# Kernel optimization log

Measured on AMD Instinct MI355X. Metric: run time of the kernel, lower is better.

## Reference

```python
import jax, jax.numpy as jnp
import numpy as np

B, S, E, H = 4, 4096, 1024, 128

def setup_inputs() -> dict:
    key = jax.random.key(0)
    kx, kk, kq, kv = jax.random.split(key, 4)
    x = jax.random.normal(kx, (B, S, E), dtype=jnp.float32)
    # torch nn.Linear weights are [out_features, in_features]
    Wk = jax.random.normal(kk, (H, E), dtype=jnp.float32) * (E ** -0.5)
    Wq = jax.random.normal(kq, (H, E), dtype=jnp.float32) * (E ** -0.5)
    Wv = jax.random.normal(kv, (H, E), dtype=jnp.float32) * (E ** -0.5)
    return {"x": x, "Wk": Wk, "Wq": Wq, "Wv": Wv}

def reference(x, Wk, Wq, Wv):
    # projections: y = x @ W.T  (bias-free nn.Linear)
    k = jnp.einsum('bse,he->bsh', x, Wk)
    q = jnp.einsum('bse,he->bsh', x, Wq)
    v = jnp.einsum('bse,he->bsh', x, Wv)
    emb = x.shape[-1]
    # scores scaled by embedding_size**-0.5 (as in the source, not head_size)
    scores = jnp.einsum('bqh,bkh->bqk', q, k) * (emb ** -0.5)  # [B,S,S]
    # causal mask: positions j > i get -inf
    i = jnp.arange(scores.shape[-2])[:, None]
    j = jnp.arange(scores.shape[-1])[None, :]
    scores = jnp.where(j > i, jnp.float32(-jnp.inf), scores)
    probs = jax.nn.softmax(scores, axis=-1)
    # dropout is identity in eval mode
    out = jnp.einsum('bqk,bkh->bqh', probs, v)  # [B,S,H]
    return out
```

## Files before the change

### kernel.cpp

```cpp
#include <hip/hip_runtime.h>

typedef short bf16x8 __attribute__((ext_vector_type(8)));
typedef float f32x4 __attribute__((ext_vector_type(4)));

#define MFMA16(a, b, c) __builtin_amdgcn_mfma_f32_16x16x32_bf16(a, b, c, 0, 0, 0)

constexpr int Bn = 4, Sn = 4096, En = 1024, Hn = 128;
constexpr float CSCALE = 1.44269504089f * 0.03125f;

__device__ inline int sb64(int qt) {
    int a = qt >> 4, r = qt & 15;
    return 8 * a * (a + 1) + r * (a + 1);
}
constexpr int SB = 160;
constexpr int SLOT_F = 8320;

__device__ inline unsigned short f2bf(float f) {
    unsigned int u = __builtin_bit_cast(unsigned int, f);
    u += 0x7fff + ((u >> 16) & 1);
    return (unsigned short)(u >> 16);
}

__device__ inline unsigned int pk2(float a, float b) {
    unsigned int ua = __builtin_bit_cast(unsigned int, a) + 0x8000u;
    unsigned int ub = __builtin_bit_cast(unsigned int, b) + 0x8000u;
    return __builtin_amdgcn_perm(ub, ua, 0x07060302u);
}

__device__ inline void gld16(const unsigned short* g, unsigned short* l) {
    __builtin_amdgcn_global_load_lds((const __attribute__((address_space(1))) void*)g,
                                     (__attribute__((address_space(3))) void*)l, 16, 0, 0);
}

__global__ __launch_bounds__(256) void prep_kernel(
    const float* __restrict__ Wk, const float* __restrict__ Wq, const float* __restrict__ Wv,
    unsigned short* __restrict__ wb, unsigned int* __restrict__ sched)
{
    int gy = blockIdx.x >> 5;
    const float* src = (gy == 0) ? Wq : (gy == 1) ? Wk : Wv;
    unsigned short* dst = wb + (size_t)gy * Hn * En;
    int t = (blockIdx.x & 31) * 256 + threadIdx.x;
    const float4* s4 = (const float4*)src;
    for (int i = 0; i < 4; ++i) {
        float4 v = s4[(size_t)t * 4 + i];
        uint2 w2 = { pk2(v.x, v.y), pk2(v.z, v.w) };
        *(uint2*)&dst[(size_t)t * 16 + i * 4] = w2;
    }
    if (blockIdx.x == 0) {
        const int bin = threadIdx.x;
        unsigned int it[4] = { 0xFFFFu, 0xFFFFu, 0xFFFFu, 0xFFFFu };
        auto fullItem = [](int k) -> unsigned int {
            int b = k / 100, j = k - 100 * b;
            int qt = 63, ch = 0;
            for (int q = 63; q >= 0; --q) {
                int f = (q + 1) >> 4;
                if (j < f) { qt = q; ch = j; break; }
                j -= f;
            }
            return (unsigned int)(qt | (ch << 6) | (b << 8));
        };
        auto remItem = [](int v, int i) -> unsigned int {
            int rep = i >> 2, b = i & 3;
            int qt = rep * 16 + v - 1, ch = rep;
            return (unsigned int)(qt | (ch << 6) | (b << 8));
        };
        if (bin < 128) {
            it[0] = fullItem(2 * bin);
            it[1] = fullItem(2 * bin + 1);
        } else if (bin < 240) {
            int t2 = bin - 128, v = 2 + (t2 >> 4), i = t2 & 15;
            it[0] = fullItem(256 + t2);
            it[1] = remItem(v, i);
            it[2] = remItem(17 - v, i);
        } else {
            int t2 = bin - 240;
            it[0] = fullItem(368 + 2 * t2);
            it[1] = fullItem(369 + 2 * t2);
            it[2] = remItem(1, t2);
        }
        for (int z = 0; z < 4; ++z) sched[z * 256 + bin] = it[z];
    }
}

__global__ __launch_bounds__(512, 2) void proj_kernel(
    const float* __restrict__ x, const unsigned short* __restrict__ wb,
    unsigned short* __restrict__ qb, unsigned short* __restrict__ kb,
    unsigned short* __restrict__ vbT)
{
    __shared__ __align__(16) unsigned short xs[2][64][64];
    __shared__ __align__(16) unsigned short wsm[2][384][64];

    const int m0 = blockIdx.x * 64;
    const int tid = threadIdx.x;
    const int lane = tid & 63, wave = tid >> 6;
    const int l15 = lane & 15, quad = lane >> 4;
    const int wn = wave * 48;

    f32x4 acc[4][3] = {};
    float4 xp[2];

    auto loadx = [&](int kc) {
        for (int p2 = 0; p2 < 2; ++p2) {
            int i = p2 * 512 + tid, row = i >> 4, c4 = (i & 15) * 4;
            xp[p2] = *(const float4*)&x[(size_t)(m0 + row) * En + kc * 64 + c4];
        }
    };
    auto writex = [&](int c) {
        for (int p2 = 0; p2 < 2; ++p2) {
            int i = p2 * 512 + tid, row = i >> 4, hc = i & 15;
            uint2 w2 = { pk2(xp[p2].x, xp[p2].y), pk2(xp[p2].z, xp[p2].w) };
            *(uint2*)((char*)&xs[c][0][0] + row * 128 + (((hc >> 1) ^ (row & 7)) << 4) + ((hc & 1) << 3)) = w2;
        }
    };
    auto issueW = [&](int kc, int c) {
        for (int j = 0; j < 6; ++j) {
            int seg = (wave * 6 + j) * 1024;
            int d = seg + (lane << 4);
            int row = d >> 7, chp = (d >> 4) & 7;
            gld16(wb + (size_t)row * En + kc * 64 + ((chp ^ (row & 7)) << 3),
                  (unsigned short*)((char*)&wsm[c][0][0] + seg));
        }
    };

    loadx(0);
    issueW(0, 0);
    writex(0);
    loadx(1);

    for (int kc = 0; kc < En / 64; ++kc) {
        const int c = kc & 1;
        __syncthreads();
        if (kc + 1 < En / 64) {
            issueW(kc + 1, c ^ 1);
            writex(c ^ 1);
            int kn = (kc + 2 < En / 64) ? kc + 2 : En / 64 - 1;
            loadx(kn);
        }
        bf16x8 xf[4][2], wf[3][2];
        for (int i = 0; i < 4; ++i)
            for (int kk = 0; kk < 2; ++kk) {
                int row = i * 16 + l15;
                int chn = (kk * 4 + quad) ^ (row & 7);
                xf[i][kk] = *(const bf16x8*)((char*)&xs[c][0][0] + row * 128 + (chn << 4));
            }
        for (int j = 0; j < 3; ++j)
            for (int kk = 0; kk < 2; ++kk) {
                int row = wn + j * 16 + l15;
                int chn = (kk * 4 + quad) ^ (row & 7);
                wf[j][kk] = *(const bf16x8*)((char*)&wsm[c][0][0] + row * 128 + (chn << 4));
            }
        for (int kk = 0; kk < 2; ++kk)
            for (int i = 0; i < 4; ++i)
                for (int j = 0; j < 3; ++j)
                    acc[i][j] = MFMA16(xf[i][kk], wf[j][kk], acc[i][j]);
    }

    for (int i = 0; i < 4; ++i) {
        int rowb = m0 + i * 16 + quad * 4;
        for (int j = 0; j < 3; ++j) {
            int gcol = wn + j * 16 + l15;
            int gy = gcol >> 7, col = gcol & 127;
            if (gy == 0) {
                for (int r = 0; r < 4; ++r)
                    qb[(size_t)(rowb + r) * Hn + col] = f2bf(acc[i][j][r] * CSCALE);
            } else if (gy == 1) {
                for (int r = 0; r < 4; ++r)
                    kb[(size_t)(rowb + r) * Hn + col] = f2bf(acc[i][j][r]);
            } else {
                int bb = rowb >> 12, ss = rowb & 4095;
                uint2 w2 = { pk2(acc[i][j][0], acc[i][j][1]), pk2(acc[i][j][2], acc[i][j][3]) };
                *(uint2*)&vbT[((size_t)(bb * 128 + col)) * Sn + ss] = w2;
            }
        }
    }
}

__global__ __launch_bounds__(256, 3) void attn_kernel(
    const unsigned short* __restrict__ qb, const unsigned short* __restrict__ kb,
    const unsigned short* __restrict__ vbT, float* __restrict__ out,
    float* __restrict__ part, const unsigned int* __restrict__ sched)
{
    __shared__ unsigned short ks[64][132];
    __shared__ unsigned short vt[128][68];
    __shared__ unsigned short ps[4][16][72];

    const unsigned int wi = sched[blockIdx.x];
    if (wi == 0xFFFFu) return;
    const int qt = (int)(wi & 63u);
    const int ch = (int)((wi >> 6) & 3u);
    const int b  = (int)((wi >> 8) & 3u);
    const int T  = qt + 1;
    const int nch = (T + 15) >> 4;
    const int t0 = ch * 16;
    const int nloc = min(16, T - t0);
    const int q0 = qt * 64;

    const int tid = threadIdx.x;
    const int lane = tid & 63, wave = tid >> 6;
    const int l15 = lane & 15, quad = lane >> 4;

    const unsigned short* qg = qb + (size_t)(b * Sn + q0) * Hn;
    bf16x8 qf[4];
    for (int f = 0; f < 4; ++f)
        qf[f] = *(const bf16x8*)&qg[(wave * 16 + l15) * Hn + f * 32 + quad * 8];

    f32x4 o[8] = {};
    float m_r = -INFINITY, l_r = 0.f;

    const unsigned short* kg = kb + (size_t)b * Sn * Hn;
    const unsigned short* vg = vbT + (size_t)b * 128 * Sn;
    unsigned short* psrow = &ps[wave][l15][0];

    bf16x8 kreg[4], vreg[4];
    auto loadKV = [&](int gt) {
        int kt0 = gt * 64;
        for (int p4 = 0; p4 < 4; ++p4) {
            int i = p4 * 256 + tid;
            kreg[p4] = *(const bf16x8*)&kg[(size_t)(kt0 + (i >> 4)) * Hn + (i & 15) * 8];
            vreg[p4] = *(const bf16x8*)&vg[(size_t)(i >> 3) * Sn + kt0 + (i & 7) * 8];
        }
    };

    loadKV(t0);
    for (int tl = 0; tl < nloc; ++tl) {
        const int gt = t0 + tl;
        for (int p4 = 0; p4 < 4; ++p4) {
            int i = p4 * 256 + tid;
            *(bf16x8*)&ks[i >> 4][(i & 15) * 8] = kreg[p4];
            *(bf16x8*)&vt[i >> 3][(i & 7) * 8] = vreg[p4];
        }
        __syncthreads();
        if (tl + 1 < nloc) loadKV(gt + 1);

        float u[4][4];
        for (int nt = 0; nt < 4; ++nt) {
            f32x4 s = {};
            for (int kk = 0; kk < 4; ++kk) {
                bf16x8 kf = *(const bf16x8*)&ks[nt * 16 + l15][kk * 32 + quad * 8];
                s = MFMA16(kf, qf[kk], s);
            }
            for (int r = 0; r < 4; ++r) u[nt][r] = s[r];
        }
        if (gt == qt) {
            int qq = wave * 16 + l15;
            for (int nt = 0; nt < 4; ++nt)
                for (int r = 0; r < 4; ++r)
                    if (nt * 16 + quad * 4 + r > qq) u[nt][r] = -INFINITY;
        }
        float mx = -INFINITY;
        for (int nt = 0; nt < 4; ++nt)
            for (int r = 0; r < 4; ++r) mx = fmaxf(mx, u[nt][r]);
        mx = fmaxf(mx, __shfl_xor(mx, 16));
        mx = fmaxf(mx, __shfl_xor(mx, 32));
        float mn = fmaxf(m_r, mx);
        float alpha = exp2f(m_r - mn);
        m_r = mn;
        float sum = 0.f;
        for (int nt = 0; nt < 4; ++nt)
            for (int r = 0; r < 4; ++r) {
                float pv = exp2f(u[nt][r] - mn);
                u[nt][r] = pv;
                sum += pv;
            }
        sum += __shfl_xor(sum, 16);
        sum += __shfl_xor(sum, 32);
        l_r = l_r * alpha + sum;

        for (int nt = 0; nt < 4; ++nt) {
            uint2 w2 = { pk2(u[nt][0], u[nt][1]), pk2(u[nt][2], u[nt][3]) };
            *(uint2*)&psrow[nt * 16 + quad * 4] = w2;
        }
        for (int t = 0; t < 8; ++t) o[t] *= alpha;

        for (int k2 = 0; k2 < 2; ++k2) {
            bf16x8 pf = *(const bf16x8*)&psrow[k2 * 32 + quad * 8];
            for (int t = 0; t < 8; ++t) {
                bf16x8 vf = *(const bf16x8*)&vt[t * 16 + l15][k2 * 32 + quad * 8];
                o[t] = MFMA16(vf, pf, o[t]);
            }
        }
        __syncthreads();
    }

    if (nch == 1) {
        float inv = 1.0f / l_r;
        float* og = out + (size_t)(b * Sn + q0 + wave * 16 + l15) * Hn;
        for (int t = 0; t < 8; ++t) {
            float4 st = { o[t][0] * inv, o[t][1] * inv, o[t][2] * inv, o[t][3] * inv };
            *(float4*)&og[t * 16 + quad * 4] = st;
        }
    } else {
        float* P = part + (size_t)(b * SB + sb64(qt) + ch) * SLOT_F;
        int q = wave * 16 + l15;
        for (int t = 0; t < 8; ++t) {
            float4 st = { o[t][0], o[t][1], o[t][2], o[t][3] };
            *(float4*)&P[q * 128 + t * 16 + quad * 4] = st;
        }
        if (quad == 0) {
            P[8192 + q] = m_r;
            P[8256 + q] = l_r;
        }
    }
}

__global__ __launch_bounds__(256) void merge_kernel(
    const float* __restrict__ part, float* __restrict__ out)
{
    const int qt = 16 + blockIdx.x;
    const int b = blockIdx.y;
    const int nch = (qt + 16) >> 4;
    const float* P0 = part + (size_t)(b * SB + sb64(qt)) * SLOT_F;
    const int q = threadIdx.x >> 2;
    const int h0 = (threadIdx.x & 3) * 32;

    float m[4], w[4];
    float M = -INFINITY;
    for (int c = 0; c < nch; ++c) {
        m[c] = P0[(size_t)c * SLOT_F + 8192 + q];
        M = fmaxf(M, m[c]);
    }
    float L = 0.f;
    for (int c = 0; c < nch; ++c) {
        w[c] = exp2f(m[c] - M);
        L += w[c] * P0[(size_t)c * SLOT_F + 8256 + q];
    }
    float inv = 1.0f / L;

    float acc[32] = {};
    for (int c = 0; c < nch; ++c) {
        const float* Pq = P0 + (size_t)c * SLOT_F + q * 128 + h0;
        for (int j = 0; j < 8; ++j) {
            float4 v = *(const float4*)&Pq[j * 4];
            acc[j * 4 + 0] += w[c] * v.x;
            acc[j * 4 + 1] += w[c] * v.y;
            acc[j * 4 + 2] += w[c] * v.z;
            acc[j * 4 + 3] += w[c] * v.w;
        }
    }
    float* og = out + (size_t)(b * Sn + qt * 64 + q) * Hn + h0;
    for (int j = 0; j < 8; ++j) {
        float4 st = { acc[j * 4 + 0] * inv, acc[j * 4 + 1] * inv,
                      acc[j * 4 + 2] * inv, acc[j * 4 + 3] * inv };
        *(float4*)&og[j * 4] = st;
    }
}

extern "C" void kernel_launch(void* const* d_in, const int* in_sizes, int n_in,
                              void* d_out, int out_size, void* d_ws, size_t ws_size,
                              hipStream_t stream)
{
    const float* x  = (const float*)d_in[0];
    const float* Wk = (const float*)d_in[1];
    const float* Wq = (const float*)d_in[2];
    const float* Wv = (const float*)d_in[3];
    float* out = (float*)d_out;

    unsigned short* qbuf  = (unsigned short*)d_ws;
    unsigned short* kbuf  = qbuf + (size_t)Bn * Sn * Hn;
    unsigned short* vbufT = kbuf + (size_t)Bn * Sn * Hn;
    unsigned short* wb    = vbufT + (size_t)Bn * Sn * Hn;
    float* part = (float*)(wb + (size_t)3 * Hn * En);
    unsigned int* sched = (unsigned int*)part;

    prep_kernel<<<96, 256, 0, stream>>>(Wk, Wq, Wv, wb, sched);
    proj_kernel<<<256, 512, 0, stream>>>(x, wb, qbuf, kbuf, vbufT);
    attn_kernel<<<1024, 256, 0, stream>>>(qbuf, kbuf, vbufT, out, part, sched);
    merge_kernel<<<dim3(48, Bn), 256, 0, stream>>>(part, out);
}
```

Measured before the change: 176.4 us.

## Split attention into 8-tile KV chunks, share LDS for K and V, raise occupancy

New measurement: 287.6 us. 1.63x slower.

```diff
diff --git a/kernel.cpp b/kernel.cpp
--- a/kernel.cpp
+++ b/kernel.cpp
@@ -8,11 +8,11 @@
 constexpr int Bn = 4, Sn = 4096, En = 1024, Hn = 128;
 constexpr float CSCALE = 1.44269504089f * 0.03125f;
 
-__device__ inline int sb64(int qt) {
-    int a = qt >> 4, r = qt & 15;
-    return 8 * a * (a + 1) + r * (a + 1);
-}
-constexpr int SB = 160;
+__device__ inline int sbase8(int qt) {
+    int a = qt >> 3, r = qt & 7;
+    return 4 * a * (a + 1) - 8 + r * (a + 1);
+}
+constexpr int NSLOT = 280;
 constexpr int SLOT_F = 8320;
 
 __device__ inline unsigned short f2bf(float f) {
@@ -48,37 +48,33 @@
     }
     if (blockIdx.x == 0) {
         const int bin = threadIdx.x;
-        unsigned int it[4] = { 0xFFFFu, 0xFFFFu, 0xFFFFu, 0xFFFFu };
-        auto fullItem = [](int k) -> unsigned int {
-            int b = k / 100, j = k - 100 * b;
+        unsigned int it[5] = { 0xFFFFu, 0xFFFFu, 0xFFFFu, 0xFFFFu, 0xFFFFu };
+        auto fullItem = [](int F) -> unsigned int {
+            int b = F / 232, j = F % 232;
             int qt = 63, ch = 0;
             for (int q = 63; q >= 0; --q) {
-                int f = (q + 1) >> 4;
-                if (j < f) { qt = q; ch = j; break; }
-                j -= f;
-            }
-            return (unsigned int)(qt | (ch << 6) | (b << 8));
+                int nf = (q + 1) >> 3;
+                if (j < nf) { qt = q; ch = j; break; }
+                j -= nf;
+            }
+            return (unsigned int)(qt | (ch << 6) | (b << 9));
         };
-        auto remItem = [](int v, int i) -> unsigned int {
-            int rep = i >> 2, b = i & 3;
-            int qt = rep * 16 + v - 1, ch = rep;
-            return (unsigned int)(qt | (ch << 6) | (b << 8));
+        auto remItem = [](int r, int i) -> unsigned int {
+            int b = i >> 3, m = i & 7;
+            int qt = 8 * m + r - 1, ch = m;
+            return (unsigned int)(qt | (ch << 6) | (b << 9));
         };
-        if (bin < 128) {
-            it[0] = fullItem(2 * bin);
-            it[1] = fullItem(2 * bin + 1);
-        } else if (bin < 240) {
-            int t2 = bin - 128, v = 2 + (t2 >> 4), i = t2 & 15;
-            it[0] = fullItem(256 + t2);
-            it[1] = remItem(v, i);
-            it[2] = remItem(17 - v, i);
+        if (bin < 160) {
+            for (int z = 0; z < 4; ++z) it[z] = fullItem(bin * 4 + z);
+            if (bin < 32) it[4] = remItem(1, bin);
         } else {
-            int t2 = bin - 240;
-            it[0] = fullItem(368 + 2 * t2);
-            it[1] = fullItem(369 + 2 * t2);
-            it[2] = remItem(1, t2);
-        }
-        for (int z = 0; z < 4; ++z) sched[z * 256 + bin] = it[z];
+            int t2 = bin - 160;
+            for (int z = 0; z < 3; ++z) it[z] = fullItem(640 + t2 * 3 + z);
+            int p = t2 >> 5, i = t2 & 31;
+            it[3] = remItem(7 - p, i);
+            it[4] = remItem(2 + p, i);
+        }
+        for (int z = 0; z < 5; ++z) sched[z * 256 + bin] = it[z];
     }
 }
 
@@ -175,24 +171,23 @@
     }
 }
 
-__global__ __launch_bounds__(256, 3) void attn_kernel(
+__global__ __launch_bounds__(256, 5) void attn_kernel(
     const unsigned short* __restrict__ qb, const unsigned short* __restrict__ kb,
     const unsigned short* __restrict__ vbT, float* __restrict__ out,
     float* __restrict__ part, const unsigned int* __restrict__ sched)
 {
-    __shared__ unsigned short ks[64][132];
-    __shared__ unsigned short vt[128][68];
+    __shared__ __align__(16) unsigned short kv[8704];
     __shared__ unsigned short ps[4][16][72];
 
     const unsigned int wi = sched[blockIdx.x];
     if (wi == 0xFFFFu) return;
     const int qt = (int)(wi & 63u);
-    const int ch = (int)((wi >> 6) & 3u);
-    const int b  = (int)((wi >> 8) & 3u);
+    const int ch = (int)((wi >> 6) & 7u);
+    const int b  = (int)((wi >> 9) & 3u);
     const int T  = qt + 1;
-    const int nch = (T + 15) >> 4;
-    const int t0 = ch * 16;
-    const int nloc = min(16, T - t0);
+    const int nch = (T + 7) >> 3;
+    const int t0 = ch * 8;
+    const int nloc = min(8, T - t0);
     const int q0 = qt * 64;
 
     const int tid = threadIdx.x;
@@ -212,31 +207,37 @@
     unsigned short* psrow = &ps[wave][l15][0];
 
     bf16x8 kreg[4], vreg[4];
-    auto loadKV = [&](int gt) {
+    auto loadK = [&](int gt) {
         int kt0 = gt * 64;
         for (int p4 = 0; p4 < 4; ++p4) {
             int i = p4 * 256 + tid;
             kreg[p4] = *(const bf16x8*)&kg[(size_t)(kt0 + (i >> 4)) * Hn + (i & 15) * 8];
+        }
+    };
+    auto loadV = [&](int gt) {
+        int kt0 = gt * 64;
+        for (int p4 = 0; p4 < 4; ++p4) {
+            int i = p4 * 256 + tid;
             vreg[p4] = *(const bf16x8*)&vg[(size_t)(i >> 3) * Sn + kt0 + (i & 7) * 8];
         }
     };
 
-    loadKV(t0);
+    loadK(t0);
+    loadV(t0);
     for (int tl = 0; tl < nloc; ++tl) {
         const int gt = t0 + tl;
         for (int p4 = 0; p4 < 4; ++p4) {
             int i = p4 * 256 + tid;
-            *(bf16x8*)&ks[i >> 4][(i & 15) * 8] = kreg[p4];
-            *(bf16x8*)&vt[i >> 3][(i & 7) * 8] = vreg[p4];
-        }
-        __syncthreads();
-        if (tl + 1 < nloc) loadKV(gt + 1);
+            *(bf16x8*)&kv[(i >> 4) * 132 + (i & 15) * 8] = kreg[p4];
+        }
+        __syncthreads();
+        if (tl + 1 < nloc) loadK(gt + 1);
 
         float u[4][4];
         for (int nt = 0; nt < 4; ++nt) {
             f32x4 s = {};
             for (int kk = 0; kk < 4; ++kk) {
-                bf16x8 kf = *(const bf16x8*)&ks[nt * 16 + l15][kk * 32 + quad * 8];
+                bf16x8 kf = *(const bf16x8*)&kv[(nt * 16 + l15) * 132 + kk * 32 + quad * 8];
                 s = MFMA16(kf, qf[kk], s);
             }
             for (int r = 0; r < 4; ++r) u[nt][r] = s[r];
@@ -265,17 +266,25 @@
         sum += __shfl_xor(sum, 16);
         sum += __shfl_xor(sum, 32);
         l_r = l_r * alpha + sum;
+        __syncthreads();
+
+        for (int p4 = 0; p4 < 4; ++p4) {
+            int i = p4 * 256 + tid;
+            *(bf16x8*)&kv[(i >> 3) * 68 + (i & 7) * 8] = vreg[p4];
+        }
+        if (tl + 1 < nloc) loadV(gt + 1);
 
         for (int nt = 0; nt < 4; ++nt) {
             uint2 w2 = { pk2(u[nt][0], u[nt][1]), pk2(u[nt][2], u[nt][3]) };
             *(uint2*)&psrow[nt * 16 + quad * 4] = w2;
         }
         for (int t = 0; t < 8; ++t) o[t] *= alpha;
+        __syncthreads();
 
         for (int k2 = 0; k2 < 2; ++k2) {
             bf16x8 pf = *(const bf16x8*)&psrow[k2 * 32 + quad * 8];
             for (int t = 0; t < 8; ++t) {
-                bf16x8 vf = *(const bf16x8*)&vt[t * 16 + l15][k2 * 32 + quad * 8];
+                bf16x8 vf = *(const bf16x8*)&kv[(t * 16 + l15) * 68 + k2 * 32 + quad * 8];
                 o[t] = MFMA16(vf, pf, o[t]);
             }
         }
@@ -290,7 +299,7 @@
             *(float4*)&og[t * 16 + quad * 4] = st;
         }
     } else {
-        float* P = part + (size_t)(b * SB + sb64(qt) + ch) * SLOT_F;
+        float* P = part + (size_t)(b * NSLOT + sbase8(qt) + ch) * SLOT_F;
         int q = wave * 16 + l15;
         for (int t = 0; t < 8; ++t) {
             float4 st = { o[t][0], o[t][1], o[t][2], o[t][3] };
@@ -306,14 +315,14 @@
 __global__ __launch_bounds__(256) void merge_kernel(
     const float* __restrict__ part, float* __restrict__ out)
 {
-    const int qt = 16 + blockIdx.x;
+    const int qt = 8 + blockIdx.x;
     const int b = blockIdx.y;
-    const int nch = (qt + 16) >> 4;
-    const float* P0 = part + (size_t)(b * SB + sb64(qt)) * SLOT_F;
+    const int nch = (qt + 8) >> 3;
+    const float* P0 = part + (size_t)(b * NSLOT + sbase8(qt)) * SLOT_F;
     const int q = threadIdx.x >> 2;
     const int h0 = (threadIdx.x & 3) * 32;
 
-    float m[4], w[4];
+    float m[8], w[8];
     float M = -INFINITY;
     for (int c = 0; c < nch; ++c) {
         m[c] = P0[(size_t)c * SLOT_F + 8192 + q];
@@ -359,11 +368,11 @@
     unsigned short* kbuf  = qbuf + (size_t)Bn * Sn * Hn;
     unsigned short* vbufT = kbuf + (size_t)Bn * Sn * Hn;
     unsigned short* wb    = vbufT + (size_t)Bn * Sn * Hn;
-    float* part = (float*)(wb + (size_t)3 * Hn * En);
-    unsigned int* sched = (unsigned int*)part;
+    unsigned int* sched   = (unsigned int*)(wb + (size_t)3 * Hn * En);
+    float* part = (float*)(sched + 2048);
 
     prep_kernel<<<96, 256, 0, stream>>>(Wk, Wq, Wv, wb, sched);
     proj_kernel<<<256, 512, 0, stream>>>(x, wb, qbuf, kbuf, vbufT);
-    attn_kernel<<<1024, 256, 0, stream>>>(qbuf, kbuf, vbufT, out, part, sched);
-    merge_kernel<<<dim3(48, Bn), 256, 0, stream>>>(part, out);
-}
+    attn_kernel<<<1280, 256, 0, stream>>>(qbuf, kbuf, vbufT, out, part, sched);
+    merge_kernel<<<dim3(56, Bn), 256, 0, stream>>>(part, out);
+}
```
